# Kernel optimization log

Measured on AMD Instinct MI355X. Metric: run time of the kernel, lower is better.

The kernel has to match this reference:

```python
import jax, jax.numpy as jnp
import numpy as np

# ---- static problem dims (mirror the Triton kernel's constexprs) ----
NUM_SEQS = 2
LQ = 1024            # query tokens per sequence (uniform varlen instance)
HIST = 1024          # cached-prefix length per sequence
LK = LQ + HIST       # total kv length per sequence
NUM_HEADS = 32
NUM_KV_HEADS = 8
HEAD_DIM = 128
BLOCK_SIZE = 64
MAX_NUM_BLOCKS = LK // BLOCK_SIZE          # 32 logical blocks per sequence
TOTAL_BLOCKS = NUM_SEQS * MAX_NUM_BLOCKS   # physical blocks in the cache
NEG = -1e10                                # matches kernel's -10000000000.0


def setup_inputs() -> dict:
    key = jax.random.key(0)
    k1, k2, k3, k4 = jax.random.split(key, 4)
    q = jax.random.normal(k1, (NUM_SEQS * LQ, NUM_HEADS, HEAD_DIM), jnp.float32)
    k_cache = jax.random.normal(k2, (TOTAL_BLOCKS, BLOCK_SIZE, NUM_KV_HEADS, HEAD_DIM), jnp.float32)
    v_cache = jax.random.normal(k3, (TOTAL_BLOCKS, BLOCK_SIZE, NUM_KV_HEADS, HEAD_DIM), jnp.float32)
    cu_seqlens_q = (jnp.arange(NUM_SEQS + 1, dtype=jnp.int32) * LQ)
    cu_seqlens_k = (jnp.arange(NUM_SEQS + 1, dtype=jnp.int32) * LK)
    # scattered physical block layout: a random permutation -> irregular gather
    block_tables = jax.random.permutation(k4, TOTAL_BLOCKS).astype(jnp.int32).reshape(NUM_SEQS, MAX_NUM_BLOCKS)
    return dict(q=q, k_cache=k_cache, v_cache=v_cache,
                cu_seqlens_q=cu_seqlens_q, cu_seqlens_k=cu_seqlens_k,
                block_tables=block_tables)


def _paged_prefill_attention(q, k_cache, v_cache, cu_seqlens_q, cu_seqlens_k, block_tables):
    scale = 1.0 / np.sqrt(HEAD_DIM)
    seq_len_q = cu_seqlens_q[1:] - cu_seqlens_q[:-1]            # [S]
    seq_len_k = cu_seqlens_k[1:] - cu_seqlens_k[:-1]            # [S]
    history_len = seq_len_k - seq_len_q                          # [S]

    # uniform varlen instance: flat [total_q, H, D] -> [S, LQ, H, D]
    qr = q.reshape(NUM_SEQS, LQ, NUM_HEADS, HEAD_DIM)
    group = NUM_HEADS // NUM_KV_HEADS
    # [S, LQ, KVH, G, D] so head h maps to kv head h // group (kernel's kv_head_idx)
    q5 = qr.reshape(NUM_SEQS, LQ, NUM_KV_HEADS, group, HEAD_DIM) * scale

    # block-table gather: logical kv layout per sequence
    safe_tables = jnp.maximum(block_tables, 0)
    k = k_cache[safe_tables].reshape(NUM_SEQS, LK, NUM_KV_HEADS, HEAD_DIM)
    v = v_cache[safe_tables].reshape(NUM_SEQS, LK, NUM_KV_HEADS, HEAD_DIM)

    # scores [S, KVH, G, LQ, LK]
    scores = jnp.einsum('sqhgd,skhd->shgqk', q5, k)

    pos_q = jnp.arange(LQ, dtype=jnp.int32)[None, :] + history_len[:, None]   # [S, LQ] absolute positions
    pos_k = jnp.arange(LK, dtype=jnp.int32)                                   # [LK]
    valid_k = (pos_k[None, :] < seq_len_k[:, None]) & \
              jnp.repeat(block_tables >= 0, BLOCK_SIZE, axis=1)               # [S, LK]
    causal = pos_q[:, :, None] >= pos_k[None, None, :]                        # [S, LQ, LK]
    mask = causal & valid_k[:, None, :]
    scores = jnp.where(mask[:, None, None, :, :], scores, NEG)

    p = jax.nn.softmax(scores, axis=-1)  # online-softmax in kernel == exact softmax
    out = jnp.einsum('shgqk,skhd->sqhgd', p, v)
    return out.reshape(NUM_SEQS * LQ, NUM_HEADS, HEAD_DIM)


def reference(q, k_cache, v_cache, cu_seqlens_q, cu_seqlens_k, block_tables):
    return _paged_prefill_attention(q, k_cache, v_cache, cu_seqlens_q, cu_seqlens_k, block_tables)
```

## Files before the change

kernel.cpp:

```cpp
#include <hip/hip_runtime.h>
#include <hip/hip_bf16.h>

#define NS_    2
#define LQ_    1024
#define HIST_  1024
#define LK_    2048
#define NH_    32
#define NKVH_  8
#define HD_    128
#define BS_    64
#define BM_    128
#define MAXB_  32

typedef __attribute__((ext_vector_type(8))) short short8;
typedef __attribute__((ext_vector_type(4))) float f32x4;

#define VSTR 72

static __device__ __forceinline__ unsigned short f2bf(float x) {
    __hip_bfloat16 h = __float2bfloat16(x);
    return *(unsigned short*)&h;
}

static __device__ __forceinline__ void cp16(const void* g, void* l) {
    __builtin_amdgcn_global_load_lds(
        (const __attribute__((address_space(1))) void*)g,
        (__attribute__((address_space(3))) void*)l, 16, 0, 0);
}

template<int CTRL>
static __device__ __forceinline__ float dppmax(float x) {
    int y = __builtin_amdgcn_update_dpp(0, __float_as_int(x), CTRL, 0xf, 0xf, true);
    return fmaxf(x, __int_as_float(y));
}

__global__ __launch_bounds__(256)
void prep_kv(const float* __restrict__ kc, const float* __restrict__ vc,
             const int* __restrict__ bt,
             unsigned short* __restrict__ Kb, unsigned short* __restrict__ Vb)
{
    __shared__ __align__(16) unsigned short Vt[HD_ * VSTR];
    const int tid = threadIdx.x;
    const int gid = blockIdx.x;
    const int seq = gid >> 8;
    const int kvh = (gid >> 5) & 7;
    const int blk = gid & 31;
    const int ph  = bt[seq * MAXB_ + blk];
    const size_t src = ((size_t)ph * BS_ * NKVH_ + kvh) * HD_;
    const int grp = seq * NKVH_ + kvh;
    const int t8 = tid >> 5, q32 = tid & 31;

    float4 kr[8], vr[8];
#pragma unroll
    for (int p = 0; p < 8; ++p)
        kr[p] = *(const float4*)(kc + src + (size_t)(p * 8 + t8) * (NKVH_ * HD_) + q32 * 4);
#pragma unroll
    for (int j = 0; j < 8; ++j)
        vr[j] = *(const float4*)(vc + src + (size_t)(t8 * 8 + j) * (NKVH_ * HD_) + q32 * 4);

#pragma unroll
    for (int p = 0; p < 8; ++p) {
        unsigned short u[4] = {f2bf(kr[p].x), f2bf(kr[p].y), f2bf(kr[p].z), f2bf(kr[p].w)};
        *(uint2*)(Kb + ((size_t)grp * LK_ + blk * BS_ + p * 8 + t8) * HD_ + q32 * 4) = *(const uint2*)u;
    }
#pragma unroll
    for (int w2 = 0; w2 < 4; ++w2) {
        unsigned short row[8];
#pragma unroll
        for (int j = 0; j < 8; ++j) {
            float f = (w2 == 0) ? vr[j].x : (w2 == 1) ? vr[j].y : (w2 == 2) ? vr[j].z : vr[j].w;
            row[j] = f2bf(f);
        }
        *(short8*)&Vt[(q32 * 4 + w2) * VSTR + t8 * 8] = *(const short8*)row;
    }
    __syncthreads();
#pragma unroll
    for (int u = 0; u < 4; ++u) {
        const int c  = tid + 256 * u;
        const int d  = c >> 3, ch = c & 7;
        uint4 x = *(const uint4*)&Vt[d * VSTR + ch * 8];
        *(uint4*)(Vb + ((size_t)grp * HD_ + d) * LK_ + blk * BS_ + ch * 8) = x;
    }
}

template<bool PREP>
__global__ __launch_bounds__(256, 2)
void paged_attn(const float* __restrict__ q,
                const unsigned short* __restrict__ Kb,
                const unsigned short* __restrict__ Vb,
                const float* __restrict__ kc,
                const float* __restrict__ vc,
                const int* __restrict__ bt,
                float* __restrict__ out)
{
    __shared__ __align__(16) unsigned short Ksh[2][BS_ * HD_];
    __shared__ __align__(16) unsigned short Vsh[2][HD_ * BS_];
    __shared__ __align__(16) unsigned short Psh[BM_ * BS_];

    const int tid  = threadIdx.x;
    const int w    = tid >> 6;
    const int lane = tid & 63;
    const int n    = lane & 15;
    const int q4   = lane >> 4;

    const int gid  = blockIdx.x;
    const int kvh  = gid & 7;
    const int slot = gid >> 3;
    const int seq  = slot >> 5;
    const int sub  = slot & 31;
    const int e    = sub & 1;
    const int t3   = (sub >> 1) & 7;
    const int hp   = sub >> 4;
    const int head = kvh * 4 + hp * 2 + e;
    const int m0   = (e ? (7 - t3) : t3) * BM_;
    const int r0   = m0 + w * 32;
    const int grp  = seq * NKVH_ + kvh;

    const float SC = 0.08838834764831845f * 1.4426950408889634f;
    short8 qf[2][4];
#pragma unroll
    for (int rt = 0; rt < 2; ++rt) {
        const size_t base = ((size_t)((seq * LQ_ + r0 + rt * 16 + n) * NH_ + head)) * HD_;
#pragma unroll
        for (int c = 0; c < 4; ++c) {
            float4 a = *(const float4*)(q + base + c * 32 + q4 * 8);
            float4 b = *(const float4*)(q + base + c * 32 + q4 * 8 + 4);
            unsigned short u[8] = {f2bf(a.x * SC), f2bf(a.y * SC), f2bf(a.z * SC), f2bf(a.w * SC),
                                   f2bf(b.x * SC), f2bf(b.y * SC), f2bf(b.z * SC), f2bf(b.w * SC)};
            qf[rt][c] = *(const short8*)u;
        }
    }

    f32x4 acc[2][8];
    f32x4 lf[2];
    float mrow[2][4];
#pragma unroll
    for (int rt = 0; rt < 2; ++rt) {
        lf[rt] = (f32x4){0.f, 0.f, 0.f, 0.f};
#pragma unroll
        for (int dt = 0; dt < 8; ++dt) acc[rt][dt] = (f32x4){0.f, 0.f, 0.f, 0.f};
#pragma unroll
        for (int r = 0; r < 4; ++r) mrow[rt][r] = -1e30f;
    }

    const int nb = (HIST_ + m0 + BM_ - 1) / BS_ + 1;
    const unsigned short* kSrc = Kb + (size_t)grp * LK_ * HD_;
    const unsigned short* vSrc = Vb + (size_t)grp * HD_ * LK_;

    const int krow_ = w * 16 + (lane >> 4);
    const int kc8_  = ((lane & 15) ^ (krow_ & 15));
    const int vd_   = w * 32 + (lane >> 3);
    const int vc8_  = ((lane & 7) ^ (vd_ & 7));

    auto issue = [&](int b, int buf) {
#pragma unroll
        for (int j = 0; j < 4; ++j) {
            const int row = krow_ + j * 4;
            const int c8  = (lane & 15) ^ (row & 15);
            cp16(kSrc + ((size_t)b * BS_ + row) * HD_ + c8 * 8, &Ksh[buf][(w * 16 + j * 4) * HD_]);
        }
#pragma unroll
        for (int j = 0; j < 4; ++j) {
            const int d  = vd_ + j * 8;
            const int c8 = (lane & 7) ^ (d & 7);
            cp16(vSrc + (size_t)d * LK_ + b * BS_ + c8 * 8, &Vsh[buf][(w * 32 + j * 8) * BS_]);
        }
    };

    if constexpr (PREP) issue(0, 0);
    short8 ones;
#pragma unroll
    for (int j = 0; j < 8; ++j) ones[j] = (short)0x3F80;

    for (int b = 0; b < nb; ++b) {
        const int cur = PREP ? (b & 1) : 0;
        __syncthreads();
        if constexpr (PREP) {
            if (b + 1 < nb) issue(b + 1, 1 ^ cur);
        } else {
            const int ph = bt[seq * MAXB_ + b];
            const size_t src = ((size_t)ph * BS_ * NKVH_ + kvh) * HD_;
#pragma unroll
            for (int j = 0; j < 4; ++j) {
                const int row = w * 16 + j * 4 + (lane >> 4);
                const int c8  = (lane & 15) ^ (row & 15);
                float4 a = *(const float4*)(kc + src + (size_t)row * (NKVH_ * HD_) + c8 * 8);
                float4 b2 = *(const float4*)(kc + src + (size_t)row * (NKVH_ * HD_) + c8 * 8 + 4);
                unsigned short u[8] = {f2bf(a.x), f2bf(a.y), f2bf(a.z), f2bf(a.w),
                                       f2bf(b2.x), f2bf(b2.y), f2bf(b2.z), f2bf(b2.w)};
                *(short8*)&Ksh[0][row * HD_ + (lane & 15) * 8] = *(const short8*)u;
            }
#pragma unroll
            for (int j = 0; j < 4; ++j) {
                const int d  = w * 32 + j * 8 + (lane >> 3);
                const int c8 = (lane & 7) ^ (d & 7);
                unsigned short u[8];
#pragma unroll
                for (int i2 = 0; i2 < 8; ++i2)
                    u[i2] = f2bf(vc[src + (size_t)(c8 * 8 + i2) * (NKVH_ * HD_) + d]);
                *(short8*)&Vsh[0][d * BS_ + (lane & 7) * 8] = *(const short8*)u;
            }
            __syncthreads();
        }

        if (64 * b <= HIST_ + r0 + 31) {
            f32x4 s[2][4];
#pragma unroll
            for (int rt = 0; rt < 2; ++rt)
#pragma unroll
                for (int kt = 0; kt < 4; ++kt) s[rt][kt] = (f32x4){0.f, 0.f, 0.f, 0.f};
#pragma unroll
            for (int kt = 0; kt < 4; ++kt) {
#pragma unroll
                for (int c = 0; c < 4; ++c) {
                    short8 kf = *(const short8*)&Ksh[cur][(kt * 16 + n) * HD_ + (((c * 4 + q4) ^ n) << 3)];
#pragma unroll
                    for (int rt = 0; rt < 2; ++rt)
                        s[rt][kt] = __builtin_amdgcn_mfma_f32_16x16x32_bf16(qf[rt][c], kf, s[rt][kt], 0, 0, 0);
                }
            }
            const bool needMask = (64 * b + 63 > HIST_ + r0);
#pragma unroll
            for (int rt = 0; rt < 2; ++rt) {
                float mx[4], al[4];
#pragma unroll
                for (int r = 0; r < 4; ++r) mx[r] = -1e30f;
#pragma unroll
                for (int kt = 0; kt < 4; ++kt) {
#pragma unroll
                    for (int r = 0; r < 4; ++r) {
                        float t = s[rt][kt][r];
                        if (needMask) {
                            const int key = b * 64 + kt * 16 + n;
                            const int row = r0 + rt * 16 + q4 * 4 + r;
                            if (key > HIST_ + row) t = -1e30f;
                        }
                        s[rt][kt][r] = t;
                        mx[r] = fmaxf(mx[r], t);
                    }
                }
#pragma unroll
                for (int r = 0; r < 4; ++r) {
                    mx[r] = dppmax<0xB1>(mx[r]);
                    mx[r] = dppmax<0x4E>(mx[r]);
                    mx[r] = dppmax<0x124>(mx[r]);
                    mx[r] = dppmax<0x128>(mx[r]);
                    const float mn = fmaxf(mrow[rt][r], mx[r]);
                    al[r] = __builtin_amdgcn_exp2f(mrow[rt][r] - mn);
                    mrow[rt][r] = mn;
                }
                const int rbase = w * 32 + rt * 16 + q4 * 4;
#pragma unroll
                for (int kt = 0; kt < 4; ++kt) {
                    const int cb = kt * 2 + (n >> 3);
                    const int ci = n & 7;
#pragma unroll
                    for (int r = 0; r < 4; ++r) {
                        const int row = rbase + r;
                        const float p = __builtin_amdgcn_exp2f(s[rt][kt][r] - mrow[rt][r]);
                        Psh[row * BS_ + ((cb ^ (row & 7)) << 3) + ci] = f2bf(p);
                    }
                }
                if (__any(al[0] != 1.f || al[1] != 1.f || al[2] != 1.f || al[3] != 1.f)) {
#pragma unroll
                    for (int dt = 0; dt < 8; ++dt)
#pragma unroll
                        for (int r = 0; r < 4; ++r) acc[rt][dt][r] *= al[r];
#pragma unroll
                    for (int r = 0; r < 4; ++r) lf[rt][r] *= al[r];
                }
            }
#pragma unroll
            for (int ks = 0; ks < 2; ++ks) {
                short8 pa[2];
#pragma unroll
                for (int rt = 0; rt < 2; ++rt)
                    pa[rt] = *(const short8*)&Psh[(w * 32 + rt * 16 + n) * BS_ + (((ks * 4 + q4) ^ (n & 7)) << 3)];
#pragma unroll
                for (int rt = 0; rt < 2; ++rt)
                    lf[rt] = __builtin_amdgcn_mfma_f32_16x16x32_bf16(pa[rt], ones, lf[rt], 0, 0, 0);
#pragma unroll
                for (int dt = 0; dt < 8; ++dt) {
                    short8 vf = *(const short8*)&Vsh[cur][(dt * 16 + n) * BS_ + (((ks * 4 + q4) ^ (n & 7)) << 3)];
#pragma unroll
                    for (int rt = 0; rt < 2; ++rt)
                        acc[rt][dt] = __builtin_amdgcn_mfma_f32_16x16x32_bf16(pa[rt], vf, acc[rt][dt], 0, 0, 0);
                }
            }
        }
    }

#pragma unroll
    for (int rt = 0; rt < 2; ++rt) {
        float rl[4];
#pragma unroll
        for (int r = 0; r < 4; ++r) rl[r] = 1.0f / lf[rt][r];
#pragma unroll
        for (int dt = 0; dt < 8; ++dt)
#pragma unroll
            for (int r = 0; r < 4; ++r) {
                const int row = r0 + rt * 16 + q4 * 4 + r;
                out[((size_t)((seq * LQ_ + row) * NH_ + head)) * HD_ + dt * 16 + n] = acc[rt][dt][r] * rl[r];
            }
    }
}

extern "C" void kernel_launch(void* const* d_in, const int* in_sizes, int n_in,
                              void* d_out, int out_size, void* d_ws, size_t ws_size,
                              hipStream_t stream) {
    const float* q  = (const float*)d_in[0];
    const float* kc = (const float*)d_in[1];
    const float* vc = (const float*)d_in[2];
    const int*   bt = (const int*)d_in[5];
    float*      out = (float*)d_out;
    (void)in_sizes; (void)n_in; (void)out_size;

    const size_t kb_elems = (size_t)NS_ * NKVH_ * LK_ * HD_;
    const size_t need = kb_elems * 2 * sizeof(unsigned short);
    if (ws_size >= need) {
        unsigned short* Kb = (unsigned short*)d_ws;
        unsigned short* Vb = Kb + kb_elems;
        prep_kv<<<512, 256, 0, stream>>>(kc, vc, bt, Kb, Vb);
        paged_attn<true><<<512, 256, 0, stream>>>(q, Kb, Vb, kc, vc, bt, out);
    } else {
        paged_attn<false><<<512, 256, 0, stream>>>(q, nullptr, nullptr, kc, vc, bt, out);
    }
}
```

Baseline: 207.9 us.

## Fuse KV bf16 conversion into attention kernel with register-prefetched fp32 loads

Drops the separate prep kernel that converted the paged fp32 K/V cache into contiguous bf16 workspace buffers. The attention kernel now gathers fp32 K/V through the block table directly into registers, prefetches the next block while computing the current one, converts to bf16 and writes swizzled single-buffered LDS. This removes a kernel launch and the workspace write/read round trip. In exchange each workgroup redoes the conversion, fp32 traffic doubles per block across many redundant CTAs, register pressure rises, and an extra barrier is added per iteration.

```diff
diff --git a/kernel.cpp b/kernel.cpp
--- a/kernel.cpp
+++ b/kernel.cpp
@@ -15,17 +15,9 @@
 typedef __attribute__((ext_vector_type(8))) short short8;
 typedef __attribute__((ext_vector_type(4))) float f32x4;
 
-#define VSTR 72
-
 static __device__ __forceinline__ unsigned short f2bf(float x) {
     __hip_bfloat16 h = __float2bfloat16(x);
     return *(unsigned short*)&h;
-}
-
-static __device__ __forceinline__ void cp16(const void* g, void* l) {
-    __builtin_amdgcn_global_load_lds(
-        (const __attribute__((address_space(1))) void*)g,
-        (__attribute__((address_space(3))) void*)l, 16, 0, 0);
 }
 
 template<int CTRL>
@@ -34,67 +26,15 @@
     return fmaxf(x, __int_as_float(y));
 }
 
-__global__ __launch_bounds__(256)
-void prep_kv(const float* __restrict__ kc, const float* __restrict__ vc,
-             const int* __restrict__ bt,
-             unsigned short* __restrict__ Kb, unsigned short* __restrict__ Vb)
-{
-    __shared__ __align__(16) unsigned short Vt[HD_ * VSTR];
-    const int tid = threadIdx.x;
-    const int gid = blockIdx.x;
-    const int seq = gid >> 8;
-    const int kvh = (gid >> 5) & 7;
-    const int blk = gid & 31;
-    const int ph  = bt[seq * MAXB_ + blk];
-    const size_t src = ((size_t)ph * BS_ * NKVH_ + kvh) * HD_;
-    const int grp = seq * NKVH_ + kvh;
-    const int t8 = tid >> 5, q32 = tid & 31;
-
-    float4 kr[8], vr[8];
-#pragma unroll
-    for (int p = 0; p < 8; ++p)
-        kr[p] = *(const float4*)(kc + src + (size_t)(p * 8 + t8) * (NKVH_ * HD_) + q32 * 4);
-#pragma unroll
-    for (int j = 0; j < 8; ++j)
-        vr[j] = *(const float4*)(vc + src + (size_t)(t8 * 8 + j) * (NKVH_ * HD_) + q32 * 4);
-
-#pragma unroll
-    for (int p = 0; p < 8; ++p) {
-        unsigned short u[4] = {f2bf(kr[p].x), f2bf(kr[p].y), f2bf(kr[p].z), f2bf(kr[p].w)};
-        *(uint2*)(Kb + ((size_t)grp * LK_ + blk * BS_ + p * 8 + t8) * HD_ + q32 * 4) = *(const uint2*)u;
-    }
-#pragma unroll
-    for (int w2 = 0; w2 < 4; ++w2) {
-        unsigned short row[8];
-#pragma unroll
-        for (int j = 0; j < 8; ++j) {
-            float f = (w2 == 0) ? vr[j].x : (w2 == 1) ? vr[j].y : (w2 == 2) ? vr[j].z : vr[j].w;
-            row[j] = f2bf(f);
-        }
-        *(short8*)&Vt[(q32 * 4 + w2) * VSTR + t8 * 8] = *(const short8*)row;
-    }
-    __syncthreads();
-#pragma unroll
-    for (int u = 0; u < 4; ++u) {
-        const int c  = tid + 256 * u;
-        const int d  = c >> 3, ch = c & 7;
-        uint4 x = *(const uint4*)&Vt[d * VSTR + ch * 8];
-        *(uint4*)(Vb + ((size_t)grp * HD_ + d) * LK_ + blk * BS_ + ch * 8) = x;
-    }
-}
-
-template<bool PREP>
 __global__ __launch_bounds__(256, 2)
 void paged_attn(const float* __restrict__ q,
-                const unsigned short* __restrict__ Kb,
-                const unsigned short* __restrict__ Vb,
                 const float* __restrict__ kc,
                 const float* __restrict__ vc,
                 const int* __restrict__ bt,
                 float* __restrict__ out)
 {
-    __shared__ __align__(16) unsigned short Ksh[2][BS_ * HD_];
-    __shared__ __align__(16) unsigned short Vsh[2][HD_ * BS_];
+    __shared__ __align__(16) unsigned short Ksh[BS_ * HD_];
+    __shared__ __align__(16) unsigned short Vsh[HD_ * BS_];
     __shared__ __align__(16) unsigned short Psh[BM_ * BS_];
 
     const int tid  = threadIdx.x;
@@ -114,7 +54,6 @@
     const int head = kvh * 4 + hp * 2 + e;
     const int m0   = (e ? (7 - t3) : t3) * BM_;
     const int r0   = m0 + w * 32;
-    const int grp  = seq * NKVH_ + kvh;
 
     const float SC = 0.08838834764831845f * 1.4426950408889634f;
     short8 qf[2][4];
@@ -143,65 +82,53 @@
         for (int r = 0; r < 4; ++r) mrow[rt][r] = -1e30f;
     }
 
-    const int nb = (HIST_ + m0 + BM_ - 1) / BS_ + 1;
-    const unsigned short* kSrc = Kb + (size_t)grp * LK_ * HD_;
-    const unsigned short* vSrc = Vb + (size_t)grp * HD_ * LK_;
-
-    const int krow_ = w * 16 + (lane >> 4);
-    const int kc8_  = ((lane & 15) ^ (krow_ & 15));
-    const int vd_   = w * 32 + (lane >> 3);
-    const int vc8_  = ((lane & 7) ^ (vd_ & 7));
-
-    auto issue = [&](int b, int buf) {
-#pragma unroll
-        for (int j = 0; j < 4; ++j) {
-            const int row = krow_ + j * 4;
-            const int c8  = (lane & 15) ^ (row & 15);
-            cp16(kSrc + ((size_t)b * BS_ + row) * HD_ + c8 * 8, &Ksh[buf][(w * 16 + j * 4) * HD_]);
-        }
-#pragma unroll
-        for (int j = 0; j < 4; ++j) {
-            const int d  = vd_ + j * 8;
-            const int c8 = (lane & 7) ^ (d & 7);
-            cp16(vSrc + (size_t)d * LK_ + b * BS_ + c8 * 8, &Vsh[buf][(w * 32 + j * 8) * BS_]);
-        }
+    const int nb  = (HIST_ + m0 + BM_ - 1) / BS_ + 1;
+    const int t8  = tid >> 5;
+    const int q32 = tid & 31;
+    const int* btp = bt + seq * MAXB_;
+
+    float4 kr[8], vr[8];
+    auto load_blk = [&](int b) {
+        const int ph = btp[b];
+        const size_t src = ((size_t)ph * BS_ * NKVH_ + kvh) * HD_;
+#pragma unroll
+        for (int p = 0; p < 8; ++p)
+            kr[p] = *(const float4*)(kc + src + (size_t)(p * 8 + t8) * (NKVH_ * HD_) + q32 * 4);
+#pragma unroll
+        for (int j = 0; j < 8; ++j)
+            vr[j] = *(const float4*)(vc + src + (size_t)(t8 * 8 + j) * (NKVH_ * HD_) + q32 * 4);
     };
-
-    if constexpr (PREP) issue(0, 0);
+    auto store_blk = [&]() {
+#pragma unroll
+        for (int p = 0; p < 8; ++p) {
+            const int row = p * 8 + t8;
+            unsigned short u[4] = {f2bf(kr[p].x), f2bf(kr[p].y), f2bf(kr[p].z), f2bf(kr[p].w)};
+            *(uint2*)&Ksh[row * HD_ + (((q32 >> 1) ^ (row & 15)) << 3) + (q32 & 1) * 4] = *(const uint2*)u;
+        }
+#pragma unroll
+        for (int w2 = 0; w2 < 4; ++w2) {
+            const int d = q32 * 4 + w2;
+            unsigned short row8[8];
+#pragma unroll
+            for (int j = 0; j < 8; ++j) {
+                float f = (w2 == 0) ? vr[j].x : (w2 == 1) ? vr[j].y : (w2 == 2) ? vr[j].z : vr[j].w;
+                row8[j] = f2bf(f);
+            }
+            const int ch = t8 ^ (d & 7) ^ ((d >> 3) & 7);
+            *(short8*)&Vsh[d * BS_ + ch * 8] = *(const short8*)row8;
+        }
+    };
+
+    load_blk(0);
     short8 ones;
 #pragma unroll
     for (int j = 0; j < 8; ++j) ones[j] = (short)0x3F80;
 
     for (int b = 0; b < nb; ++b) {
-        const int cur = PREP ? (b & 1) : 0;
         __syncthreads();
-        if constexpr (PREP) {
-            if (b + 1 < nb) issue(b + 1, 1 ^ cur);
-        } else {
-            const int ph = bt[seq * MAXB_ + b];
-            const size_t src = ((size_t)ph * BS_ * NKVH_ + kvh) * HD_;
-#pragma unroll
-            for (int j = 0; j < 4; ++j) {
-                const int row = w * 16 + j * 4 + (lane >> 4);
-                const int c8  = (lane & 15) ^ (row & 15);
-                float4 a = *(const float4*)(kc + src + (size_t)row * (NKVH_ * HD_) + c8 * 8);
-                float4 b2 = *(const float4*)(kc + src + (size_t)row * (NKVH_ * HD_) + c8 * 8 + 4);
-                unsigned short u[8] = {f2bf(a.x), f2bf(a.y), f2bf(a.z), f2bf(a.w),
-                                       f2bf(b2.x), f2bf(b2.y), f2bf(b2.z), f2bf(b2.w)};
-                *(short8*)&Ksh[0][row * HD_ + (lane & 15) * 8] = *(const short8*)u;
-            }
-#pragma unroll
-            for (int j = 0; j < 4; ++j) {
-                const int d  = w * 32 + j * 8 + (lane >> 3);
-                const int c8 = (lane & 7) ^ (d & 7);
-                unsigned short u[8];
-#pragma unroll
-                for (int i2 = 0; i2 < 8; ++i2)
-                    u[i2] = f2bf(vc[src + (size_t)(c8 * 8 + i2) * (NKVH_ * HD_) + d]);
-                *(short8*)&Vsh[0][d * BS_ + (lane & 7) * 8] = *(const short8*)u;
-            }
-            __syncthreads();
-        }
+        store_blk();
+        __syncthreads();
+        if (b + 1 < nb) load_blk(b + 1);
 
         if (64 * b <= HIST_ + r0 + 31) {
             f32x4 s[2][4];
@@ -213,7 +140,7 @@
             for (int kt = 0; kt < 4; ++kt) {
 #pragma unroll
                 for (int c = 0; c < 4; ++c) {
-                    short8 kf = *(const short8*)&Ksh[cur][(kt * 16 + n) * HD_ + (((c * 4 + q4) ^ n) << 3)];
+                    short8 kf = *(const short8*)&Ksh[(kt * 16 + n) * HD_ + (((c * 4 + q4) ^ n) << 3)];
 #pragma unroll
                     for (int rt = 0; rt < 2; ++rt)
                         s[rt][kt] = __builtin_amdgcn_mfma_f32_16x16x32_bf16(qf[rt][c], kf, s[rt][kt], 0, 0, 0);
@@ -281,7 +208,8 @@
                     lf[rt] = __builtin_amdgcn_mfma_f32_16x16x32_bf16(pa[rt], ones, lf[rt], 0, 0, 0);
 #pragma unroll
                 for (int dt = 0; dt < 8; ++dt) {
-                    short8 vf = *(const short8*)&Vsh[cur][(dt * 16 + n) * BS_ + (((ks * 4 + q4) ^ (n & 7)) << 3)];
+                    const int d = dt * 16 + n;
+                    short8 vf = *(const short8*)&Vsh[d * BS_ + ((((ks * 4 + q4) ^ (d & 7) ^ ((d >> 3) & 7))) << 3)];
 #pragma unroll
                     for (int rt = 0; rt < 2; ++rt)
                         acc[rt][dt] = __builtin_amdgcn_mfma_f32_16x16x32_bf16(pa[rt], vf, acc[rt][dt], 0, 0, 0);
@@ -313,16 +241,7 @@
     const float* vc = (const float*)d_in[2];
     const int*   bt = (const int*)d_in[5];
     float*      out = (float*)d_out;
-    (void)in_sizes; (void)n_in; (void)out_size;
-
-    const size_t kb_elems = (size_t)NS_ * NKVH_ * LK_ * HD_;
-    const size_t need = kb_elems * 2 * sizeof(unsigned short);
-    if (ws_size >= need) {
-        unsigned short* Kb = (unsigned short*)d_ws;
-        unsigned short* Vb = Kb + kb_elems;
-        prep_kv<<<512, 256, 0, stream>>>(kc, vc, bt, Kb, Vb);
-        paged_attn<true><<<512, 256, 0, stream>>>(q, Kb, Vb, kc, vc, bt, out);
-    } else {
-        paged_attn<false><<<512, 256, 0, stream>>>(q, nullptr, nullptr, kc, vc, bt, out);
-    }
-}
+    (void)in_sizes; (void)n_in; (void)out_size; (void)d_ws; (void)ws_size;
+
+    paged_attn<<<512, 256, 0, stream>>>(q, kc, vc, bt, out);
+}
```

New measurement: 406.4 us. +95.5%, slower.

## Load K/V MFMA fragments directly from global into registers, drop LDS staging

Applied to the files above, without the earlier changes.

Removes the shared-memory double buffers for K and V. Each wave now loads its MFMA fragments straight from global (L2) into a 16-entry register buffer that alternates between K and V, with per-wave trip counts and no block-wide barriers. P conversion to bf16 is changed from round-to-nearest to truncation. This trades LDS traffic and syncs for duplicated global loads across the four waves and exposed load latency, since K for the next block is loaded only after PV finishes.

```diff
diff --git a/kernel.cpp b/kernel.cpp
--- a/kernel.cpp
+++ b/kernel.cpp
@@ -20,12 +20,6 @@
 static __device__ __forceinline__ unsigned short f2bf(float x) {
     __hip_bfloat16 h = __float2bfloat16(x);
     return *(unsigned short*)&h;
-}
-
-static __device__ __forceinline__ void cp16(const void* g, void* l) {
-    __builtin_amdgcn_global_load_lds(
-        (const __attribute__((address_space(1))) void*)g,
-        (__attribute__((address_space(3))) void*)l, 16, 0, 0);
 }
 
 template<int CTRL>
@@ -93,8 +87,6 @@
                 const int* __restrict__ bt,
                 float* __restrict__ out)
 {
-    __shared__ __align__(16) unsigned short Ksh[2][BS_ * HD_];
-    __shared__ __align__(16) unsigned short Vsh[2][HD_ * BS_];
     __shared__ __align__(16) unsigned short Psh[BM_ * BS_];
 
     const int tid  = threadIdx.x;
@@ -143,151 +135,152 @@
         for (int r = 0; r < 4; ++r) mrow[rt][r] = -1e30f;
     }
 
-    const int nb = (HIST_ + m0 + BM_ - 1) / BS_ + 1;
+    const int nb_w = ((HIST_ + r0 + 31) >> 6) + 1;
     const unsigned short* kSrc = Kb + (size_t)grp * LK_ * HD_;
     const unsigned short* vSrc = Vb + (size_t)grp * HD_ * LK_;
-
-    const int krow_ = w * 16 + (lane >> 4);
-    const int kc8_  = ((lane & 15) ^ (krow_ & 15));
-    const int vd_   = w * 32 + (lane >> 3);
-    const int vc8_  = ((lane & 7) ^ (vd_ & 7));
-
-    auto issue = [&](int b, int buf) {
-#pragma unroll
-        for (int j = 0; j < 4; ++j) {
-            const int row = krow_ + j * 4;
-            const int c8  = (lane & 15) ^ (row & 15);
-            cp16(kSrc + ((size_t)b * BS_ + row) * HD_ + c8 * 8, &Ksh[buf][(w * 16 + j * 4) * HD_]);
-        }
-#pragma unroll
-        for (int j = 0; j < 4; ++j) {
-            const int d  = vd_ + j * 8;
-            const int c8 = (lane & 7) ^ (d & 7);
-            cp16(vSrc + (size_t)d * LK_ + b * BS_ + c8 * 8, &Vsh[buf][(w * 32 + j * 8) * BS_]);
+    const int* btp = bt + seq * MAXB_;
+
+    short8 fbuf[16];
+
+    auto loadK = [&](int b) {
+        if constexpr (PREP) {
+            const unsigned short* base = kSrc + (size_t)b * BS_ * HD_ + n * HD_ + q4 * 8;
+#pragma unroll
+            for (int kt = 0; kt < 4; ++kt)
+#pragma unroll
+                for (int c = 0; c < 4; ++c)
+                    fbuf[kt * 4 + c] = *(const short8*)(base + kt * 16 * HD_ + c * 32);
+        } else {
+            const int ph = btp[b];
+            const size_t src = ((size_t)ph * BS_ * NKVH_ + kvh) * HD_;
+#pragma unroll
+            for (int kt = 0; kt < 4; ++kt)
+#pragma unroll
+                for (int c = 0; c < 4; ++c) {
+                    const float* p4 = kc + src + (size_t)(kt * 16 + n) * (NKVH_ * HD_) + c * 32 + q4 * 8;
+                    float4 a = *(const float4*)p4;
+                    float4 d = *(const float4*)(p4 + 4);
+                    unsigned short u[8] = {f2bf(a.x), f2bf(a.y), f2bf(a.z), f2bf(a.w),
+                                           f2bf(d.x), f2bf(d.y), f2bf(d.z), f2bf(d.w)};
+                    fbuf[kt * 4 + c] = *(const short8*)u;
+                }
         }
     };
-
-    if constexpr (PREP) issue(0, 0);
+    auto loadV = [&](int b) {
+        if constexpr (PREP) {
+            const unsigned short* base = vSrc + (size_t)n * LK_ + b * BS_ + q4 * 8;
+#pragma unroll
+            for (int ks = 0; ks < 2; ++ks)
+#pragma unroll
+                for (int dt = 0; dt < 8; ++dt)
+                    fbuf[ks * 8 + dt] = *(const short8*)(base + (size_t)dt * 16 * LK_ + ks * 32);
+        } else {
+            const int ph = btp[b];
+            const size_t src = ((size_t)ph * BS_ * NKVH_ + kvh) * HD_;
+#pragma unroll
+            for (int ks = 0; ks < 2; ++ks)
+#pragma unroll
+                for (int dt = 0; dt < 8; ++dt) {
+                    unsigned short u[8];
+#pragma unroll
+                    for (int j = 0; j < 8; ++j)
+                        u[j] = f2bf(vc[src + (size_t)(ks * 32 + q4 * 8 + j) * (NKVH_ * HD_) + dt * 16 + n]);
+                    fbuf[ks * 8 + dt] = *(const short8*)u;
+                }
+        }
+    };
+
+    loadK(0);
     short8 ones;
 #pragma unroll
     for (int j = 0; j < 8; ++j) ones[j] = (short)0x3F80;
 
-    for (int b = 0; b < nb; ++b) {
-        const int cur = PREP ? (b & 1) : 0;
-        __syncthreads();
-        if constexpr (PREP) {
-            if (b + 1 < nb) issue(b + 1, 1 ^ cur);
-        } else {
-            const int ph = bt[seq * MAXB_ + b];
-            const size_t src = ((size_t)ph * BS_ * NKVH_ + kvh) * HD_;
-#pragma unroll
-            for (int j = 0; j < 4; ++j) {
-                const int row = w * 16 + j * 4 + (lane >> 4);
-                const int c8  = (lane & 15) ^ (row & 15);
-                float4 a = *(const float4*)(kc + src + (size_t)row * (NKVH_ * HD_) + c8 * 8);
-                float4 b2 = *(const float4*)(kc + src + (size_t)row * (NKVH_ * HD_) + c8 * 8 + 4);
-                unsigned short u[8] = {f2bf(a.x), f2bf(a.y), f2bf(a.z), f2bf(a.w),
-                                       f2bf(b2.x), f2bf(b2.y), f2bf(b2.z), f2bf(b2.w)};
-                *(short8*)&Ksh[0][row * HD_ + (lane & 15) * 8] = *(const short8*)u;
-            }
-#pragma unroll
-            for (int j = 0; j < 4; ++j) {
-                const int d  = w * 32 + j * 8 + (lane >> 3);
-                const int c8 = (lane & 7) ^ (d & 7);
-                unsigned short u[8];
-#pragma unroll
-                for (int i2 = 0; i2 < 8; ++i2)
-                    u[i2] = f2bf(vc[src + (size_t)(c8 * 8 + i2) * (NKVH_ * HD_) + d]);
-                *(short8*)&Vsh[0][d * BS_ + (lane & 7) * 8] = *(const short8*)u;
-            }
-            __syncthreads();
-        }
-
-        if (64 * b <= HIST_ + r0 + 31) {
-            f32x4 s[2][4];
+    for (int b = 0; b < nb_w; ++b) {
+        f32x4 s[2][4];
+#pragma unroll
+        for (int rt = 0; rt < 2; ++rt)
+#pragma unroll
+            for (int kt = 0; kt < 4; ++kt) s[rt][kt] = (f32x4){0.f, 0.f, 0.f, 0.f};
+#pragma unroll
+        for (int kt = 0; kt < 4; ++kt)
+#pragma unroll
+            for (int c = 0; c < 4; ++c) {
+                const short8 kf = fbuf[kt * 4 + c];
+#pragma unroll
+                for (int rt = 0; rt < 2; ++rt)
+                    s[rt][kt] = __builtin_amdgcn_mfma_f32_16x16x32_bf16(qf[rt][c], kf, s[rt][kt], 0, 0, 0);
+            }
+        loadV(b);
+
+        const bool needMask = (64 * b + 63 > HIST_ + r0);
+#pragma unroll
+        for (int rt = 0; rt < 2; ++rt) {
+            float mx[4], al[4];
+#pragma unroll
+            for (int r = 0; r < 4; ++r) mx[r] = -1e30f;
+#pragma unroll
+            for (int kt = 0; kt < 4; ++kt)
+#pragma unroll
+                for (int r = 0; r < 4; ++r) {
+                    float t = s[rt][kt][r];
+                    if (needMask) {
+                        const int key = b * 64 + kt * 16 + n;
+                        const int row = r0 + rt * 16 + q4 * 4 + r;
+                        if (key > HIST_ + row) t = -1e30f;
+                    }
+                    s[rt][kt][r] = t;
+                    mx[r] = fmaxf(mx[r], t);
+                }
+#pragma unroll
+            for (int r = 0; r < 4; ++r) {
+                mx[r] = dppmax<0xB1>(mx[r]);
+                mx[r] = dppmax<0x4E>(mx[r]);
+                mx[r] = dppmax<0x124>(mx[r]);
+                mx[r] = dppmax<0x128>(mx[r]);
+                const float mn = fmaxf(mrow[rt][r], mx[r]);
+                al[r] = __builtin_amdgcn_exp2f(mrow[rt][r] - mn);
+                mrow[rt][r] = mn;
+            }
+            const int rbase = w * 32 + rt * 16 + q4 * 4;
+#pragma unroll
+            for (int kt = 0; kt < 4; ++kt) {
+                const int cb = kt * 2 + (n >> 3);
+                const int ci = n & 7;
+#pragma unroll
+                for (int r = 0; r < 4; ++r) {
+                    const int row = rbase + r;
+                    const float p = __builtin_amdgcn_exp2f(s[rt][kt][r] - mrow[rt][r]);
+                    Psh[row * BS_ + ((cb ^ (row & 7)) << 3) + ci] =
+                        (unsigned short)(__float_as_uint(p) >> 16);
+                }
+            }
+            if (__any(al[0] != 1.f || al[1] != 1.f || al[2] != 1.f || al[3] != 1.f)) {
+#pragma unroll
+                for (int dt = 0; dt < 8; ++dt)
+#pragma unroll
+                    for (int r = 0; r < 4; ++r) acc[rt][dt][r] *= al[r];
+#pragma unroll
+                for (int r = 0; r < 4; ++r) lf[rt][r] *= al[r];
+            }
+        }
+#pragma unroll
+        for (int ks = 0; ks < 2; ++ks) {
+            short8 pa[2];
 #pragma unroll
             for (int rt = 0; rt < 2; ++rt)
-#pragma unroll
-                for (int kt = 0; kt < 4; ++kt) s[rt][kt] = (f32x4){0.f, 0.f, 0.f, 0.f};
-#pragma unroll
-            for (int kt = 0; kt < 4; ++kt) {
-#pragma unroll
-                for (int c = 0; c < 4; ++c) {
-                    short8 kf = *(const short8*)&Ksh[cur][(kt * 16 + n) * HD_ + (((c * 4 + q4) ^ n) << 3)];
-#pragma unroll
-                    for (int rt = 0; rt < 2; ++rt)
-                        s[rt][kt] = __builtin_amdgcn_mfma_f32_16x16x32_bf16(qf[rt][c], kf, s[rt][kt], 0, 0, 0);
-                }
-            }
-            const bool needMask = (64 * b + 63 > HIST_ + r0);
-#pragma unroll
-            for (int rt = 0; rt < 2; ++rt) {
-                float mx[4], al[4];
-#pragma unroll
-                for (int r = 0; r < 4; ++r) mx[r] = -1e30f;
-#pragma unroll
-                for (int kt = 0; kt < 4; ++kt) {
-#pragma unroll
-                    for (int r = 0; r < 4; ++r) {
-                        float t = s[rt][kt][r];
-                        if (needMask) {
-                            const int key = b * 64 + kt * 16 + n;
-                            const int row = r0 + rt * 16 + q4 * 4 + r;
-                            if (key > HIST_ + row) t = -1e30f;
-                        }
-                        s[rt][kt][r] = t;
-                        mx[r] = fmaxf(mx[r], t);
-                    }
-                }
-#pragma unroll
-                for (int r = 0; r < 4; ++r) {
-                    mx[r] = dppmax<0xB1>(mx[r]);
-                    mx[r] = dppmax<0x4E>(mx[r]);
-                    mx[r] = dppmax<0x124>(mx[r]);
-                    mx[r] = dppmax<0x128>(mx[r]);
-                    const float mn = fmaxf(mrow[rt][r], mx[r]);
-                    al[r] = __builtin_amdgcn_exp2f(mrow[rt][r] - mn);
-                    mrow[rt][r] = mn;
-                }
-                const int rbase = w * 32 + rt * 16 + q4 * 4;
-#pragma unroll
-                for (int kt = 0; kt < 4; ++kt) {
-                    const int cb = kt * 2 + (n >> 3);
-                    const int ci = n & 7;
-#pragma unroll
-                    for (int r = 0; r < 4; ++r) {
-                        const int row = rbase + r;
-                        const float p = __builtin_amdgcn_exp2f(s[rt][kt][r] - mrow[rt][r]);
-                        Psh[row * BS_ + ((cb ^ (row & 7)) << 3) + ci] = f2bf(p);
-                    }
-                }
-                if (__any(al[0] != 1.f || al[1] != 1.f || al[2] != 1.f || al[3] != 1.f)) {
-#pragma unroll
-                    for (int dt = 0; dt < 8; ++dt)
-#pragma unroll
-                        for (int r = 0; r < 4; ++r) acc[rt][dt][r] *= al[r];
-#pragma unroll
-                    for (int r = 0; r < 4; ++r) lf[rt][r] *= al[r];
-                }
-            }
-#pragma unroll
-            for (int ks = 0; ks < 2; ++ks) {
-                short8 pa[2];
+                pa[rt] = *(const short8*)&Psh[(w * 32 + rt * 16 + n) * BS_ + (((ks * 4 + q4) ^ (n & 7)) << 3)];
+#pragma unroll
+            for (int rt = 0; rt < 2; ++rt)
+                lf[rt] = __builtin_amdgcn_mfma_f32_16x16x32_bf16(pa[rt], ones, lf[rt], 0, 0, 0);
+#pragma unroll
+            for (int dt = 0; dt < 8; ++dt) {
+                const short8 vf = fbuf[ks * 8 + dt];
 #pragma unroll
                 for (int rt = 0; rt < 2; ++rt)
-                    pa[rt] = *(const short8*)&Psh[(w * 32 + rt * 16 + n) * BS_ + (((ks * 4 + q4) ^ (n & 7)) << 3)];
-#pragma unroll
-                for (int rt = 0; rt < 2; ++rt)
-                    lf[rt] = __builtin_amdgcn_mfma_f32_16x16x32_bf16(pa[rt], ones, lf[rt], 0, 0, 0);
-#pragma unroll
-                for (int dt = 0; dt < 8; ++dt) {
-                    short8 vf = *(const short8*)&Vsh[cur][(dt * 16 + n) * BS_ + (((ks * 4 + q4) ^ (n & 7)) << 3)];
-#pragma unroll
-                    for (int rt = 0; rt < 2; ++rt)
-                        acc[rt][dt] = __builtin_amdgcn_mfma_f32_16x16x32_bf16(pa[rt], vf, acc[rt][dt], 0, 0, 0);
-                }
-            }
-        }
+                    acc[rt][dt] = __builtin_amdgcn_mfma_f32_16x16x32_bf16(pa[rt], vf, acc[rt][dt], 0, 0, 0);
+            }
+        }
+        if (b + 1 < nb_w) loadK(b + 1);
     }
 
 #pragma unroll
```

New measurement: 391.0 us. +88.0%, slower.
